# Kernel tuning notes

Measured on AMD Instinct MI355X. Metric: run time of the kernel, lower is better.

Reference implementation:

```python
import jax, jax.numpy as jnp
import numpy as np

B, T, E, H = 2, 4096, 1024, 16
D = E // H  # head dim = 64

def setup_inputs() -> dict:
    key = jax.random.key(0)
    ks = jax.random.split(key, 5)
    x = jax.random.normal(ks[0], (B, T, E), dtype=jnp.float32)
    # torch Linear(n_embed, 3*n_embed): y = x @ W.T + b ; we store W already transposed as (E, 3E)
    w_qkv = jax.random.normal(ks[1], (E, 3 * E), dtype=jnp.float32) * (1.0 / np.sqrt(E))
    b_qkv = jax.random.normal(ks[2], (3 * E,), dtype=jnp.float32) * 0.02
    w_out = jax.random.normal(ks[3], (E, E), dtype=jnp.float32) * (1.0 / np.sqrt(E))
    b_out = jax.random.normal(ks[4], (E,), dtype=jnp.float32) * 0.02
    return {"x": x, "w_qkv": w_qkv, "b_qkv": b_qkv, "w_out": w_out, "b_out": b_out}

def reference(x, w_qkv, b_qkv, w_out, b_out):
    b, t, e = x.shape
    qkv = x @ w_qkv + b_qkv                      # (B,T,3E)
    # matches torch: view(B,T,H,3D) then chunk(3, dim=-1)
    qkv = qkv.reshape(b, t, H, 3 * D)
    q, k, v = jnp.split(qkv, 3, axis=-1)          # each (B,T,H,D)
    q = q.transpose(0, 2, 1, 3)                   # (B,H,T,D)
    k = k.transpose(0, 2, 1, 3)
    v = v.transpose(0, 2, 1, 3)
    scores = jnp.einsum('bhqd,bhkd->bhqk', q, k) / jnp.sqrt(jnp.float32(D))
    causal = jnp.tril(jnp.ones((t, t), dtype=bool))
    scores = jnp.where(causal, scores, jnp.float32(-jnp.inf))
    w = jax.nn.softmax(scores, axis=-1)           # (B,H,T,T)
    out = jnp.einsum('bhqk,bhkd->bhqd', w, v)     # (B,H,T,D)
    out = out.transpose(0, 2, 1, 3).reshape(b, t, e)
    return out @ w_out + b_out
```

## Files before the change

### kernel.cpp

```cpp
#include <hip/hip_runtime.h>
#include <stdint.h>
#include <math.h>

#define T_SEQ 4096

typedef __attribute__((ext_vector_type(8))) short short8;
typedef __attribute__((ext_vector_type(4))) float f32x4;
typedef __attribute__((ext_vector_type(4))) uint16_t u16x4;

__device__ __forceinline__ uint16_t f2bf(float f) {
  uint32_t u = __float_as_uint(f);
  u += 0x7FFFu + ((u >> 16) & 1u);
  return (uint16_t)(u >> 16);
}

__device__ __forceinline__ void gload_lds16(const uint16_t* g, uint16_t* l) {
  __builtin_amdgcn_global_load_lds(
      (const __attribute__((address_space(1))) void*)g,
      (__attribute__((address_space(3))) void*)l, 16, 0, 0);
}

__global__ void __launch_bounds__(256) k_cvt(const float* __restrict__ in,
                                             uint16_t* __restrict__ out, int n4) {
  int i = blockIdx.x * 256 + threadIdx.x;
  if (i >= n4) return;
  float4 v = reinterpret_cast<const float4*>(in)[i];
  u16x4 o = { f2bf(v.x), f2bf(v.y), f2bf(v.z), f2bf(v.w) };
  reinterpret_cast<u16x4*>(out)[i] = o;
}

__global__ void __launch_bounds__(256) k_tc(const float* __restrict__ w,
                                            uint16_t* __restrict__ wt, int R, int C) {
  __shared__ uint16_t tile[32][33];
  int tx = threadIdx.x & 31, ty = threadIdx.x >> 5;
  int r0 = blockIdx.y * 32, c0 = blockIdx.x * 32;
#pragma unroll
  for (int i = 0; i < 4; i++)
    tile[ty + 8 * i][tx] = f2bf(w[(size_t)(r0 + ty + 8 * i) * C + c0 + tx]);
  __syncthreads();
#pragma unroll
  for (int i = 0; i < 4; i++)
    wt[(size_t)(c0 + ty + 8 * i) * R + r0 + tx] = tile[tx][ty + 8 * i];
}

__global__ void __launch_bounds__(256) k_vt(const uint16_t* __restrict__ qkv,
                                            uint16_t* __restrict__ vT) {
  __shared__ uint16_t tile[64][65];
  const int bh = blockIdx.y, b = bh >> 4, h = bh & 15;
  const int t0 = blockIdx.x * 64;
  const int tid = threadIdx.x;
  const int r = tid >> 3, c8 = tid & 7;
  const uint16_t* src = qkv + ((size_t)b * T_SEQ + t0) * 3072 + h * 192 + 128;
#pragma unroll
  for (int i = 0; i < 2; i++) {
    int row = r + 32 * i;
    short8 v = *reinterpret_cast<const short8*>(src + (size_t)row * 3072 + c8 * 8);
#pragma unroll
    for (int j = 0; j < 8; j++) tile[row][c8 * 8 + j] = (uint16_t)v[j];
  }
  __syncthreads();
  uint16_t* dst = vT + ((size_t)bh * 64) * T_SEQ + t0;
#pragma unroll
  for (int i = 0; i < 2; i++) {
    int d = r + 32 * i;
    short8 v;
#pragma unroll
    for (int j = 0; j < 8; j++) v[j] = (short)tile[c8 * 8 + j][d];
    *reinterpret_cast<short8*>(dst + (size_t)d * T_SEQ + c8 * 8) = v;
  }
}

template <int BF16_OUT>
__global__ void __launch_bounds__(256) k_gemm(const uint16_t* __restrict__ A,
                                              const uint16_t* __restrict__ BT,
                                              const float* __restrict__ bias,
                                              void* __restrict__ Cout,
                                              int M, int N, int K) {
  __shared__ __align__(16) uint16_t As[128][32];
  __shared__ __align__(16) uint16_t Bs[128][32];
  const int tid = threadIdx.x;
  const int lane = tid & 63, wid = tid >> 6;
  const int lr = lane & 15, lg = lane >> 4;
  const int wr = wid >> 1, wc = wid & 1;

  const int bid = blockIdx.x;
  const int cpx = gridDim.x >> 3;
  const int lin = (bid & 7) * cpx + (bid >> 3);
  const int nxt = N >> 7;
  const int m0 = (lin / nxt) * 128, n0 = (lin % nxt) * 128;

  const f32x4 vzero = {0.f, 0.f, 0.f, 0.f};
  f32x4 acc[4][4];
#pragma unroll
  for (int i = 0; i < 4; i++)
#pragma unroll
    for (int j = 0; j < 4; j++) acc[i][j] = vzero;

  const int seg0 = wid * 2;
  const int srow = lane >> 2;
  const int scol = (lane & 3) * 8;
  const uint16_t* Ag = A + (size_t)m0 * K;
  const uint16_t* Bg = BT + (size_t)n0 * K;
  const size_t ra0 = (size_t)(seg0 * 16 + srow) * K + scol;
  const size_t ra1 = (size_t)(seg0 * 16 + 16 + srow) * K + scol;

  for (int kk = 0; kk < K; kk += 32) {
    __syncthreads();
    gload_lds16(Ag + ra0 + kk, &As[seg0 * 16][0]);
    gload_lds16(Ag + ra1 + kk, &As[seg0 * 16 + 16][0]);
    gload_lds16(Bg + ra0 + kk, &Bs[seg0 * 16][0]);
    gload_lds16(Bg + ra1 + kk, &Bs[seg0 * 16 + 16][0]);
    __syncthreads();
    short8 af[4], bfr[4];
#pragma unroll
    for (int mi = 0; mi < 4; mi++)
      af[mi] = *reinterpret_cast<const short8*>(&As[wr * 64 + mi * 16 + lr][lg * 8]);
#pragma unroll
    for (int nj = 0; nj < 4; nj++)
      bfr[nj] = *reinterpret_cast<const short8*>(&Bs[wc * 64 + nj * 16 + lr][lg * 8]);
#pragma unroll
    for (int mi = 0; mi < 4; mi++)
#pragma unroll
      for (int nj = 0; nj < 4; nj++)
        acc[mi][nj] = __builtin_amdgcn_mfma_f32_16x16x32_bf16(af[mi], bfr[nj], acc[mi][nj], 0, 0, 0);
  }

#pragma unroll
  for (int nj = 0; nj < 4; nj++) {
    int col = n0 + wc * 64 + nj * 16 + lr;
    float bv = bias[col];
#pragma unroll
    for (int mi = 0; mi < 4; mi++) {
      int rowb = m0 + wr * 64 + mi * 16 + lg * 4;
#pragma unroll
      for (int r = 0; r < 4; r++) {
        float v = acc[mi][nj][r] + bv;
        if (BF16_OUT)
          ((uint16_t*)Cout)[(size_t)(rowb + r) * N + col] = f2bf(v);
        else
          ((float*)Cout)[(size_t)(rowb + r) * N + col] = v;
      }
    }
  }
}

#define KVB 64
__global__ void __launch_bounds__(256) k_attn(const uint16_t* __restrict__ qkv,
                                              const uint16_t* __restrict__ vT,
                                              uint16_t* __restrict__ out) {
  __shared__ __align__(16) char lds[24576];
  char* ksb = lds;
  char* vsb = lds + 8192;
  const int tid = threadIdx.x;
  const int lane = tid & 63, wid = tid >> 6;
  const int lr = lane & 15, lg = lane >> 4;
  char* psb = lds + 16384 + wid * 2048;

  const int bid = blockIdx.x;
  const int xcd = bid & 7, j = bid >> 3;
  const int bh = xcd * 4 + (j & 3);
  const int qt = 31 - (j >> 2);
  const int b = bh >> 4, h = bh & 15;
  const int q0 = qt * 128;
  const size_t rowbase = (size_t)b * T_SEQ;
  const int hoff = h * 192;
  const uint16_t* Kg = qkv + rowbase * 3072 + hoff + 64;
  const uint16_t* Vg = vT + (size_t)bh * 64 * T_SEQ;

  const int sr = tid >> 3, sc = tid & 7;
  const int wsw = (sc ^ (sr & 7)) * 16;
  const int swz = (lr & 7) << 4;
  const float C_SC = 0.180336881f;
  const float C_B = -14.4269504f;

  short8 ones8;
#pragma unroll
  for (int i = 0; i < 8; i++) ones8[i] = (lr == 0) ? (short)0x3F80 : (short)0;

  const f32x4 vzero = {0.f, 0.f, 0.f, 0.f};

  short8 qf[2][2];
#pragma unroll
  for (int qq = 0; qq < 2; qq++)
#pragma unroll
    for (int c = 0; c < 2; c++)
      qf[qq][c] = *reinterpret_cast<const short8*>(
          qkv + (rowbase + q0 + wid * 32 + qq * 16 + lr) * 3072 + hoff + c * 32 + lg * 8);

  f32x4 o[2][4];
  f32x4 o4[2];
#pragma unroll
  for (int qq = 0; qq < 2; qq++) {
    o4[qq] = vzero;
#pragma unroll
    for (int dt = 0; dt < 4; dt++) o[qq][dt] = vzero;
  }

  const int nkt = 2 * qt + 2;
  const int qwmax = q0 + wid * 32 + 31;

  short8 rk0, rk1, rv0, rv1;
  rk0 = *reinterpret_cast<const short8*>(Kg + (size_t)sr * 3072 + sc * 8);
  rk1 = *reinterpret_cast<const short8*>(Kg + (size_t)(sr + 32) * 3072 + sc * 8);
  rv0 = *reinterpret_cast<const short8*>(Vg + (size_t)sr * T_SEQ + sc * 8);
  rv1 = *reinterpret_cast<const short8*>(Vg + (size_t)(sr + 32) * T_SEQ + sc * 8);

  for (int kt = 0; kt < nkt; kt++) {
    __syncthreads();
    *reinterpret_cast<short8*>(ksb + sr * 128 + wsw) = rk0;
    *reinterpret_cast<short8*>(ksb + (sr + 32) * 128 + wsw) = rk1;
    *reinterpret_cast<short8*>(vsb + sr * 128 + wsw) = rv0;
    *reinterpret_cast<short8*>(vsb + (sr + 32) * 128 + wsw) = rv1;
    if (kt + 1 < nkt) {
      int k0n = (kt + 1) * KVB;
      rk0 = *reinterpret_cast<const short8*>(Kg + (size_t)(k0n + sr) * 3072 + sc * 8);
      rk1 = *reinterpret_cast<const short8*>(Kg + (size_t)(k0n + sr + 32) * 3072 + sc * 8);
      rv0 = *reinterpret_cast<const short8*>(Vg + (size_t)sr * T_SEQ + k0n + sc * 8);
      rv1 = *reinterpret_cast<const short8*>(Vg + (size_t)(sr + 32) * T_SEQ + k0n + sc * 8);
    }
    __syncthreads();

    if (kt * KVB <= qwmax) {
      f32x4 s0[4], s1[4];
      __builtin_amdgcn_s_setprio(1);
#pragma unroll
      for (int t = 0; t < 4; t++) {
        int row = t * 16 + lr;
        short8 kf0 = *reinterpret_cast<const short8*>(
            ksb + row * 128 + ((lg * 16) ^ swz));
        short8 kf1 = *reinterpret_cast<const short8*>(
            ksb + row * 128 + ((64 + lg * 16) ^ swz));
        s0[t] = __builtin_amdgcn_mfma_f32_16x16x32_bf16(kf0, qf[0][0], vzero, 0, 0, 0);
        s0[t] = __builtin_amdgcn_mfma_f32_16x16x32_bf16(kf1, qf[0][1], s0[t], 0, 0, 0);
        s1[t] = __builtin_amdgcn_mfma_f32_16x16x32_bf16(kf0, qf[1][0], vzero, 0, 0, 0);
        s1[t] = __builtin_amdgcn_mfma_f32_16x16x32_bf16(kf1, qf[1][1], s1[t], 0, 0, 0);
      }
      __builtin_amdgcn_s_setprio(0);
      short8 vf[4][2];
#pragma unroll
      for (int dt = 0; dt < 4; dt++)
#pragma unroll
        for (int c2 = 0; c2 < 2; c2++)
          vf[dt][c2] = *reinterpret_cast<const short8*>(
              vsb + (dt * 16 + lr) * 128 + ((c2 * 64 + lg * 16) ^ swz));

#pragma unroll
      for (int qq = 0; qq < 2; qq++) {
        f32x4* s = qq ? s1 : s0;
        const int qrow = q0 + wid * 32 + qq * 16 + lr;
        const bool notfull = (kt * KVB + 63 > q0 + wid * 32 + qq * 16);
#pragma unroll
        for (int t = 0; t < 4; t++)
#pragma unroll
          for (int r = 0; r < 4; r++) {
            float v = s[t][r];
            if (notfull) {
              int key = kt * KVB + t * 16 + lg * 4 + r;
              if (key > qrow) v = -INFINITY;
            }
            s[t][r] = __builtin_amdgcn_exp2f(v * C_SC + C_B);
          }
#pragma unroll
        for (int t = 0; t < 4; t++) {
          uint32_t w0, w1;
          asm("v_cvt_pk_bf16_f32 %0, %1, %2" : "=v"(w0) : "v"(s[t][0]), "v"(s[t][1]));
          asm("v_cvt_pk_bf16_f32 %0, %1, %2" : "=v"(w1) : "v"(s[t][2]), "v"(s[t][3]));
          uint2 ww; ww.x = w0; ww.y = w1;
          *reinterpret_cast<uint2*>(psb + lr * 128 + ((t * 32 + lg * 8) ^ swz)) = ww;
        }
        __builtin_amdgcn_s_setprio(1);
#pragma unroll
        for (int c2 = 0; c2 < 2; c2++) {
          short8 pf = *reinterpret_cast<const short8*>(
              psb + lr * 128 + ((c2 * 64 + lg * 16) ^ swz));
          o4[qq] = __builtin_amdgcn_mfma_f32_16x16x32_bf16(ones8, pf, o4[qq], 0, 0, 0);
#pragma unroll
          for (int dt = 0; dt < 4; dt++)
            o[qq][dt] = __builtin_amdgcn_mfma_f32_16x16x32_bf16(vf[dt][c2], pf, o[qq][dt], 0, 0, 0);
        }
        __builtin_amdgcn_s_setprio(0);
      }
    }
  }

  __syncthreads();
  char* scrb = lds + wid * 4096;
#pragma unroll
  for (int qq = 0; qq < 2; qq++) {
    float lsum = __shfl(o4[qq][0], lr);
    float inv = 1.0f / lsum;
#pragma unroll
    for (int dt = 0; dt < 4; dt++)
#pragma unroll
      for (int r = 0; r < 4; r++)
        *reinterpret_cast<float*>(scrb + lr * 256 + ((dt * 64 + lg * 16) ^ swz) + r * 4) =
            o[qq][dt][r] * inv;
    int row = lane >> 2, ch = lane & 3;
    uint16_t tmp[16];
#pragma unroll
    for (int k = 0; k < 4; k++) {
      f32x4 vv = *reinterpret_cast<const f32x4*>(
          scrb + row * 256 + ((ch * 64 + k * 16) ^ ((row & 7) << 4)));
#pragma unroll
      for (int j2 = 0; j2 < 4; j2++) tmp[k * 4 + j2] = f2bf(vv[j2]);
    }
    uint16_t* op = out + (rowbase + q0 + wid * 32 + qq * 16 + row) * 1024 + h * 64 + ch * 16;
    *reinterpret_cast<short8*>(op) = *reinterpret_cast<const short8*>(tmp);
    *reinterpret_cast<short8*>(op + 8) = *reinterpret_cast<const short8*>(tmp + 8);
  }
}

extern "C" void kernel_launch(void* const* d_in, const int* in_sizes, int n_in,
                              void* d_out, int out_size, void* d_ws, size_t ws_size,
                              hipStream_t stream) {
  const float* x = (const float*)d_in[0];
  const float* w_qkv = (const float*)d_in[1];
  const float* b_qkv = (const float*)d_in[2];
  const float* w_out = (const float*)d_in[3];
  const float* b_out = (const float*)d_in[4];
  float* out = (float*)d_out;

  uint8_t* ws = (uint8_t*)d_ws;
  uint16_t* x_bf  = (uint16_t*)(ws);
  uint16_t* wqkvT = (uint16_t*)(ws + (16u << 20));
  uint16_t* woutT = (uint16_t*)(ws + (22u << 20));
  uint16_t* qkv   = (uint16_t*)(ws + (24u << 20));
  uint16_t* vTbuf = (uint16_t*)(ws + (72u << 20));
  uint16_t* attn_o = x_bf;

  k_cvt<<<8192, 256, 0, stream>>>(x, x_bf, 2097152);
  k_tc<<<dim3(96, 32), 256, 0, stream>>>(w_qkv, wqkvT, 1024, 3072);
  k_tc<<<dim3(32, 32), 256, 0, stream>>>(w_out, woutT, 1024, 1024);
  k_gemm<1><<<1536, 256, 0, stream>>>(x_bf, wqkvT, b_qkv, qkv, 8192, 3072, 1024);
  k_vt<<<dim3(64, 32), 256, 0, stream>>>(qkv, vTbuf);
  k_attn<<<1024, 256, 0, stream>>>(qkv, vTbuf, attn_o);
  k_gemm<0><<<512, 256, 0, stream>>>(attn_o, woutT, b_out, out, 8192, 1024, 1024);
}
```

Before: 253.6 us.

## Load K/V fragments directly from global per wave, dropping shared LDS staging

Measured after the change: 370.8 us. 1.46x slower.

```diff
diff --git a/kernel.cpp b/kernel.cpp
--- a/kernel.cpp
+++ b/kernel.cpp
@@ -144,17 +144,14 @@
   }
 }
 
-#define KVB 64
 __global__ void __launch_bounds__(256) k_attn(const uint16_t* __restrict__ qkv,
                                               const uint16_t* __restrict__ vT,
                                               uint16_t* __restrict__ out) {
-  __shared__ __align__(16) char lds[24576];
-  char* ksb = lds;
-  char* vsb = lds + 8192;
+  __shared__ __align__(16) char lds[16384];
   const int tid = threadIdx.x;
   const int lane = tid & 63, wid = tid >> 6;
   const int lr = lane & 15, lg = lane >> 4;
-  char* psb = lds + 16384 + wid * 2048;
+  char* psb = lds + wid * 4096;
 
   const int bid = blockIdx.x;
   const int xcd = bid & 7, j = bid >> 3;
@@ -167,11 +164,8 @@
   const uint16_t* Kg = qkv + rowbase * 3072 + hoff + 64;
   const uint16_t* Vg = vT + (size_t)bh * 64 * T_SEQ;
 
-  const int sr = tid >> 3, sc = tid & 7;
-  const int wsw = (sc ^ (sr & 7)) * 16;
   const int swz = (lr & 7) << 4;
   const float C_SC = 0.180336881f;
-  const float C_B = -14.4269504f;
 
   short8 ones8;
 #pragma unroll
@@ -183,9 +177,18 @@
 #pragma unroll
   for (int qq = 0; qq < 2; qq++)
 #pragma unroll
-    for (int c = 0; c < 2; c++)
-      qf[qq][c] = *reinterpret_cast<const short8*>(
+    for (int c = 0; c < 2; c++) {
+      short8 raw = *reinterpret_cast<const short8*>(
           qkv + (rowbase + q0 + wid * 32 + qq * 16 + lr) * 3072 + hoff + c * 32 + lg * 8);
+      union { short8 s; uint32_t u[4]; } pk;
+#pragma unroll
+      for (int e = 0; e < 4; e++) {
+        float f0 = __uint_as_float(((uint32_t)(uint16_t)raw[2 * e]) << 16) * C_SC;
+        float f1 = __uint_as_float(((uint32_t)(uint16_t)raw[2 * e + 1]) << 16) * C_SC;
+        asm("v_cvt_pk_bf16_f32 %0, %1, %2" : "=v"(pk.u[e]) : "v"(f0), "v"(f1));
+      }
+      qf[qq][c] = pk.s;
+    }
 
   f32x4 o[2][4];
   f32x4 o4[2];
@@ -196,95 +199,89 @@
     for (int dt = 0; dt < 4; dt++) o[qq][dt] = vzero;
   }
 
-  const int nkt = 2 * qt + 2;
   const int qwmax = q0 + wid * 32 + 31;
-
-  short8 rk0, rk1, rv0, rv1;
-  rk0 = *reinterpret_cast<const short8*>(Kg + (size_t)sr * 3072 + sc * 8);
-  rk1 = *reinterpret_cast<const short8*>(Kg + (size_t)(sr + 32) * 3072 + sc * 8);
-  rv0 = *reinterpret_cast<const short8*>(Vg + (size_t)sr * T_SEQ + sc * 8);
-  rv1 = *reinterpret_cast<const short8*>(Vg + (size_t)(sr + 32) * T_SEQ + sc * 8);
-
-  for (int kt = 0; kt < nkt; kt++) {
-    __syncthreads();
-    *reinterpret_cast<short8*>(ksb + sr * 128 + wsw) = rk0;
-    *reinterpret_cast<short8*>(ksb + (sr + 32) * 128 + wsw) = rk1;
-    *reinterpret_cast<short8*>(vsb + sr * 128 + wsw) = rv0;
-    *reinterpret_cast<short8*>(vsb + (sr + 32) * 128 + wsw) = rv1;
-    if (kt + 1 < nkt) {
-      int k0n = (kt + 1) * KVB;
-      rk0 = *reinterpret_cast<const short8*>(Kg + (size_t)(k0n + sr) * 3072 + sc * 8);
-      rk1 = *reinterpret_cast<const short8*>(Kg + (size_t)(k0n + sr + 32) * 3072 + sc * 8);
-      rv0 = *reinterpret_cast<const short8*>(Vg + (size_t)sr * T_SEQ + k0n + sc * 8);
-      rv1 = *reinterpret_cast<const short8*>(Vg + (size_t)(sr + 32) * T_SEQ + k0n + sc * 8);
-    }
-    __syncthreads();
-
-    if (kt * KVB <= qwmax) {
-      f32x4 s0[4], s1[4];
+  const int nktw = (qwmax >> 6) + 1;
+
+  short8 kf[4][2], vf[4][2];
+#pragma unroll
+  for (int t = 0; t < 4; t++)
+#pragma unroll
+    for (int c = 0; c < 2; c++)
+      kf[t][c] = *reinterpret_cast<const short8*>(
+          Kg + (size_t)(t * 16 + lr) * 3072 + c * 32 + lg * 8);
+#pragma unroll
+  for (int dt = 0; dt < 4; dt++)
+#pragma unroll
+    for (int c2 = 0; c2 < 2; c2++)
+      vf[dt][c2] = *reinterpret_cast<const short8*>(
+          Vg + (size_t)(dt * 16 + lr) * T_SEQ + c2 * 32 + lg * 8);
+
+  for (int kt = 0; kt < nktw; kt++) {
+    f32x4 s0[4], s1[4];
+    __builtin_amdgcn_s_setprio(1);
+#pragma unroll
+    for (int t = 0; t < 4; t++) {
+      s0[t] = __builtin_amdgcn_mfma_f32_16x16x32_bf16(kf[t][0], qf[0][0], vzero, 0, 0, 0);
+      s0[t] = __builtin_amdgcn_mfma_f32_16x16x32_bf16(kf[t][1], qf[0][1], s0[t], 0, 0, 0);
+      s1[t] = __builtin_amdgcn_mfma_f32_16x16x32_bf16(kf[t][0], qf[1][0], vzero, 0, 0, 0);
+      s1[t] = __builtin_amdgcn_mfma_f32_16x16x32_bf16(kf[t][1], qf[1][1], s1[t], 0, 0, 0);
+    }
+    __builtin_amdgcn_s_setprio(0);
+    if (kt + 1 < nktw) {
+#pragma unroll
+      for (int t = 0; t < 4; t++)
+#pragma unroll
+        for (int c = 0; c < 2; c++)
+          kf[t][c] = *reinterpret_cast<const short8*>(
+              Kg + (size_t)((kt + 1) * 64 + t * 16 + lr) * 3072 + c * 32 + lg * 8);
+    }
+
+#pragma unroll
+    for (int qq = 0; qq < 2; qq++) {
+      f32x4* s = qq ? s1 : s0;
+      const int qrow = q0 + wid * 32 + qq * 16 + lr;
+      const bool notfull = (kt * 64 + 63 > q0 + wid * 32 + qq * 16);
+#pragma unroll
+      for (int t = 0; t < 4; t++)
+#pragma unroll
+        for (int r = 0; r < 4; r++) {
+          float v = s[t][r];
+          if (notfull) {
+            int key = kt * 64 + t * 16 + lg * 4 + r;
+            if (key > qrow) v = -INFINITY;
+          }
+          s[t][r] = __builtin_amdgcn_exp2f(v);
+        }
+#pragma unroll
+      for (int t = 0; t < 4; t++) {
+        uint32_t w0, w1;
+        asm("v_cvt_pk_bf16_f32 %0, %1, %2" : "=v"(w0) : "v"(s[t][0]), "v"(s[t][1]));
+        asm("v_cvt_pk_bf16_f32 %0, %1, %2" : "=v"(w1) : "v"(s[t][2]), "v"(s[t][3]));
+        uint2 ww; ww.x = w0; ww.y = w1;
+        *reinterpret_cast<uint2*>(psb + lr * 128 + ((t * 32 + lg * 8) ^ swz)) = ww;
+      }
       __builtin_amdgcn_s_setprio(1);
 #pragma unroll
-      for (int t = 0; t < 4; t++) {
-        int row = t * 16 + lr;
-        short8 kf0 = *reinterpret_cast<const short8*>(
-            ksb + row * 128 + ((lg * 16) ^ swz));
-        short8 kf1 = *reinterpret_cast<const short8*>(
-            ksb + row * 128 + ((64 + lg * 16) ^ swz));
-        s0[t] = __builtin_amdgcn_mfma_f32_16x16x32_bf16(kf0, qf[0][0], vzero, 0, 0, 0);
-        s0[t] = __builtin_amdgcn_mfma_f32_16x16x32_bf16(kf1, qf[0][1], s0[t], 0, 0, 0);
-        s1[t] = __builtin_amdgcn_mfma_f32_16x16x32_bf16(kf0, qf[1][0], vzero, 0, 0, 0);
-        s1[t] = __builtin_amdgcn_mfma_f32_16x16x32_bf16(kf1, qf[1][1], s1[t], 0, 0, 0);
+      for (int c2 = 0; c2 < 2; c2++) {
+        short8 pf = *reinterpret_cast<const short8*>(
+            psb + lr * 128 + ((c2 * 64 + lg * 16) ^ swz));
+        o4[qq] = __builtin_amdgcn_mfma_f32_16x16x32_bf16(ones8, pf, o4[qq], 0, 0, 0);
+#pragma unroll
+        for (int dt = 0; dt < 4; dt++)
+          o[qq][dt] = __builtin_amdgcn_mfma_f32_16x16x32_bf16(vf[dt][c2], pf, o[qq][dt], 0, 0, 0);
       }
       __builtin_amdgcn_s_setprio(0);
-      short8 vf[4][2];
+    }
+    if (kt + 1 < nktw) {
 #pragma unroll
       for (int dt = 0; dt < 4; dt++)
 #pragma unroll
         for (int c2 = 0; c2 < 2; c2++)
           vf[dt][c2] = *reinterpret_cast<const short8*>(
-              vsb + (dt * 16 + lr) * 128 + ((c2 * 64 + lg * 16) ^ swz));
-
-#pragma unroll
-      for (int qq = 0; qq < 2; qq++) {
-        f32x4* s = qq ? s1 : s0;
-        const int qrow = q0 + wid * 32 + qq * 16 + lr;
-        const bool notfull = (kt * KVB + 63 > q0 + wid * 32 + qq * 16);
-#pragma unroll
-        for (int t = 0; t < 4; t++)
-#pragma unroll
-          for (int r = 0; r < 4; r++) {
-            float v = s[t][r];
-            if (notfull) {
-              int key = kt * KVB + t * 16 + lg * 4 + r;
-              if (key > qrow) v = -INFINITY;
-            }
-            s[t][r] = __builtin_amdgcn_exp2f(v * C_SC + C_B);
-          }
-#pragma unroll
-        for (int t = 0; t < 4; t++) {
-          uint32_t w0, w1;
-          asm("v_cvt_pk_bf16_f32 %0, %1, %2" : "=v"(w0) : "v"(s[t][0]), "v"(s[t][1]));
-          asm("v_cvt_pk_bf16_f32 %0, %1, %2" : "=v"(w1) : "v"(s[t][2]), "v"(s[t][3]));
-          uint2 ww; ww.x = w0; ww.y = w1;
-          *reinterpret_cast<uint2*>(psb + lr * 128 + ((t * 32 + lg * 8) ^ swz)) = ww;
-        }
-        __builtin_amdgcn_s_setprio(1);
-#pragma unroll
-        for (int c2 = 0; c2 < 2; c2++) {
-          short8 pf = *reinterpret_cast<const short8*>(
-              psb + lr * 128 + ((c2 * 64 + lg * 16) ^ swz));
-          o4[qq] = __builtin_amdgcn_mfma_f32_16x16x32_bf16(ones8, pf, o4[qq], 0, 0, 0);
-#pragma unroll
-          for (int dt = 0; dt < 4; dt++)
-            o[qq][dt] = __builtin_amdgcn_mfma_f32_16x16x32_bf16(vf[dt][c2], pf, o[qq][dt], 0, 0, 0);
-        }
-        __builtin_amdgcn_s_setprio(0);
-      }
-    }
-  }
-
-  __syncthreads();
-  char* scrb = lds + wid * 4096;
+              Vg + (size_t)(dt * 16 + lr) * T_SEQ + (kt + 1) * 64 + c2 * 32 + lg * 8);
+    }
+  }
+
 #pragma unroll
   for (int qq = 0; qq < 2; qq++) {
     float lsum = __shfl(o4[qq][0], lr);
@@ -293,14 +290,14 @@
     for (int dt = 0; dt < 4; dt++)
 #pragma unroll
       for (int r = 0; r < 4; r++)
-        *reinterpret_cast<float*>(scrb + lr * 256 + ((dt * 64 + lg * 16) ^ swz) + r * 4) =
+        *reinterpret_cast<float*>(psb + lr * 256 + ((dt * 64 + lg * 16) ^ swz) + r * 4) =
             o[qq][dt][r] * inv;
     int row = lane >> 2, ch = lane & 3;
     uint16_t tmp[16];
 #pragma unroll
     for (int k = 0; k < 4; k++) {
       f32x4 vv = *reinterpret_cast<const f32x4*>(
-          scrb + row * 256 + ((ch * 64 + k * 16) ^ ((row & 7) << 4)));
+          psb + row * 256 + ((ch * 64 + k * 16) ^ ((row & 7) << 4)));
 #pragma unroll
       for (int j2 = 0; j2 < 4; j2++) tmp[k * 4 + j2] = f2bf(vv[j2]);
     }
```

## Double-buffer K/V tiles in LDS and fold softmax scale into Q

Applied to the files above, without the earlier changes.

Measured after the change: 251.7 us. About the same (-0.8%).

```diff
diff --git a/kernel.cpp b/kernel.cpp
--- a/kernel.cpp
+++ b/kernel.cpp
@@ -148,13 +148,11 @@
 __global__ void __launch_bounds__(256) k_attn(const uint16_t* __restrict__ qkv,
                                               const uint16_t* __restrict__ vT,
                                               uint16_t* __restrict__ out) {
-  __shared__ __align__(16) char lds[24576];
-  char* ksb = lds;
-  char* vsb = lds + 8192;
+  __shared__ __align__(16) char lds[40960];
   const int tid = threadIdx.x;
   const int lane = tid & 63, wid = tid >> 6;
   const int lr = lane & 15, lg = lane >> 4;
-  char* psb = lds + 16384 + wid * 2048;
+  char* psb = lds + 32768 + wid * 2048;
 
   const int bid = blockIdx.x;
   const int xcd = bid & 7, j = bid >> 3;
@@ -171,7 +169,6 @@
   const int wsw = (sc ^ (sr & 7)) * 16;
   const int swz = (lr & 7) << 4;
   const float C_SC = 0.180336881f;
-  const float C_B = -14.4269504f;
 
   short8 ones8;
 #pragma unroll
@@ -183,9 +180,18 @@
 #pragma unroll
   for (int qq = 0; qq < 2; qq++)
 #pragma unroll
-    for (int c = 0; c < 2; c++)
-      qf[qq][c] = *reinterpret_cast<const short8*>(
+    for (int c = 0; c < 2; c++) {
+      short8 raw = *reinterpret_cast<const short8*>(
           qkv + (rowbase + q0 + wid * 32 + qq * 16 + lr) * 3072 + hoff + c * 32 + lg * 8);
+      union { short8 s; uint32_t u[4]; } pk;
+#pragma unroll
+      for (int e = 0; e < 4; e++) {
+        float f0 = __uint_as_float(((uint32_t)(uint16_t)raw[2 * e]) << 16) * C_SC;
+        float f1 = __uint_as_float(((uint32_t)(uint16_t)raw[2 * e + 1]) << 16) * C_SC;
+        asm("v_cvt_pk_bf16_f32 %0, %1, %2" : "=v"(pk.u[e]) : "v"(f0), "v"(f1));
+      }
+      qf[qq][c] = pk.s;
+    }
 
   f32x4 o[2][4];
   f32x4 o4[2];
@@ -204,32 +210,53 @@
   rk1 = *reinterpret_cast<const short8*>(Kg + (size_t)(sr + 32) * 3072 + sc * 8);
   rv0 = *reinterpret_cast<const short8*>(Vg + (size_t)sr * T_SEQ + sc * 8);
   rv1 = *reinterpret_cast<const short8*>(Vg + (size_t)(sr + 32) * T_SEQ + sc * 8);
+  {
+    char* kb0 = lds;
+    char* vb0 = lds + 16384;
+    *reinterpret_cast<short8*>(kb0 + sr * 128 + wsw) = rk0;
+    *reinterpret_cast<short8*>(kb0 + (sr + 32) * 128 + wsw) = rk1;
+    *reinterpret_cast<short8*>(vb0 + sr * 128 + wsw) = rv0;
+    *reinterpret_cast<short8*>(vb0 + (sr + 32) * 128 + wsw) = rv1;
+  }
+  if (nkt > 1) {
+    rk0 = *reinterpret_cast<const short8*>(Kg + (size_t)(KVB + sr) * 3072 + sc * 8);
+    rk1 = *reinterpret_cast<const short8*>(Kg + (size_t)(KVB + sr + 32) * 3072 + sc * 8);
+    rv0 = *reinterpret_cast<const short8*>(Vg + (size_t)sr * T_SEQ + KVB + sc * 8);
+    rv1 = *reinterpret_cast<const short8*>(Vg + (size_t)(sr + 32) * T_SEQ + KVB + sc * 8);
+  }
 
   for (int kt = 0; kt < nkt; kt++) {
     __syncthreads();
-    *reinterpret_cast<short8*>(ksb + sr * 128 + wsw) = rk0;
-    *reinterpret_cast<short8*>(ksb + (sr + 32) * 128 + wsw) = rk1;
-    *reinterpret_cast<short8*>(vsb + sr * 128 + wsw) = rv0;
-    *reinterpret_cast<short8*>(vsb + (sr + 32) * 128 + wsw) = rv1;
     if (kt + 1 < nkt) {
-      int k0n = (kt + 1) * KVB;
-      rk0 = *reinterpret_cast<const short8*>(Kg + (size_t)(k0n + sr) * 3072 + sc * 8);
-      rk1 = *reinterpret_cast<const short8*>(Kg + (size_t)(k0n + sr + 32) * 3072 + sc * 8);
-      rv0 = *reinterpret_cast<const short8*>(Vg + (size_t)sr * T_SEQ + k0n + sc * 8);
-      rv1 = *reinterpret_cast<const short8*>(Vg + (size_t)(sr + 32) * T_SEQ + k0n + sc * 8);
-    }
-    __syncthreads();
+      const int nsel = (kt + 1) & 1;
+      char* kb = lds + (nsel ? 8192 : 0);
+      char* vb = lds + 16384 + (nsel ? 8192 : 0);
+      *reinterpret_cast<short8*>(kb + sr * 128 + wsw) = rk0;
+      *reinterpret_cast<short8*>(kb + (sr + 32) * 128 + wsw) = rk1;
+      *reinterpret_cast<short8*>(vb + sr * 128 + wsw) = rv0;
+      *reinterpret_cast<short8*>(vb + (sr + 32) * 128 + wsw) = rv1;
+      if (kt + 2 < nkt) {
+        int k0n = (kt + 2) * KVB;
+        rk0 = *reinterpret_cast<const short8*>(Kg + (size_t)(k0n + sr) * 3072 + sc * 8);
+        rk1 = *reinterpret_cast<const short8*>(Kg + (size_t)(k0n + sr + 32) * 3072 + sc * 8);
+        rv0 = *reinterpret_cast<const short8*>(Vg + (size_t)sr * T_SEQ + k0n + sc * 8);
+        rv1 = *reinterpret_cast<const short8*>(Vg + (size_t)(sr + 32) * T_SEQ + k0n + sc * 8);
+      }
+    }
 
     if (kt * KVB <= qwmax) {
+      const int csel = kt & 1;
+      char* kcur = lds + (csel ? 8192 : 0);
+      char* vcur = lds + 16384 + (csel ? 8192 : 0);
       f32x4 s0[4], s1[4];
       __builtin_amdgcn_s_setprio(1);
 #pragma unroll
       for (int t = 0; t < 4; t++) {
         int row = t * 16 + lr;
         short8 kf0 = *reinterpret_cast<const short8*>(
-            ksb + row * 128 + ((lg * 16) ^ swz));
+            kcur + row * 128 + ((lg * 16) ^ swz));
         short8 kf1 = *reinterpret_cast<const short8*>(
-            ksb + row * 128 + ((64 + lg * 16) ^ swz));
+            kcur + row * 128 + ((64 + lg * 16) ^ swz));
         s0[t] = __builtin_amdgcn_mfma_f32_16x16x32_bf16(kf0, qf[0][0], vzero, 0, 0, 0);
         s0[t] = __builtin_amdgcn_mfma_f32_16x16x32_bf16(kf1, qf[0][1], s0[t], 0, 0, 0);
         s1[t] = __builtin_amdgcn_mfma_f32_16x16x32_bf16(kf0, qf[1][0], vzero, 0, 0, 0);
@@ -242,7 +269,7 @@
 #pragma unroll
         for (int c2 = 0; c2 < 2; c2++)
           vf[dt][c2] = *reinterpret_cast<const short8*>(
-              vsb + (dt * 16 + lr) * 128 + ((c2 * 64 + lg * 16) ^ swz));
+              vcur + (dt * 16 + lr) * 128 + ((c2 * 64 + lg * 16) ^ swz));
 
 #pragma unroll
       for (int qq = 0; qq < 2; qq++) {
@@ -258,7 +285,7 @@
               int key = kt * KVB + t * 16 + lg * 4 + r;
               if (key > qrow) v = -INFINITY;
             }
-            s[t][r] = __builtin_amdgcn_exp2f(v * C_SC + C_B);
+            s[t][r] = __builtin_amdgcn_exp2f(v);
           }
 #pragma unroll
         for (int t = 0; t < 4; t++) {
```
